# Kernel optimization log

Hardware: AMD Instinct MI355X
Metric: run time of the kernel (lower is better)

Reference implementation:

```python
import jax, jax.numpy as jnp
import numpy as np

B, T, D, OUT = 128, 4096, 64, 512  # batch(list len), max frames, feature_size, output_size


def setup_inputs() -> dict:
    key = jax.random.key(0)
    ks = jax.random.split(key, 12)
    s = 0.05
    return {
        "x": jax.random.normal(ks[0], (B, T, D), jnp.float32),
        # true frame counts per ragged item, in [256, T]
        "lengths": jax.random.randint(ks[1], (B,), 256, T + 1, dtype=jnp.int32),
        # td1: Conv2d(1, D, (3, D)) weight [D,1,3,D], bias [D]
        "W1": jax.random.normal(ks[2], (D, 1, 3, D), jnp.float32) * s,
        "b1": jax.random.normal(ks[3], (D,), jnp.float32) * s,
        # td2: Conv2d(1, D, (1, D)) weight [D,1,1,D], bias [D]
        "W2": jax.random.normal(ks[4], (D, 1, 1, D), jnp.float32) * s,
        "b2": jax.random.normal(ks[5], (D,), jnp.float32) * s,
        # segment-level MLP: D->256->256->OUT (torch Linear layout [out,in])
        "Wl1": jax.random.normal(ks[6], (256, D), jnp.float32) * s,
        "bl1": jax.random.normal(ks[7], (256,), jnp.float32) * s,
        "Wl2": jax.random.normal(ks[8], (256, 256), jnp.float32) * s,
        "bl2": jax.random.normal(ks[9], (256,), jnp.float32) * s,
        "Wl3": jax.random.normal(ks[10], (OUT, 256), jnp.float32) * s,
        "bl3": jax.random.normal(ks[11], (OUT,), jnp.float32) * s,
    }


def reference(x, lengths, W1, b1, W2, b2, Wl1, bl1, Wl2, bl2, Wl3, bl3):
    # td1: sliding window of 3 frames, full-width feature contraction -> [B, T-2, F]
    # (avoid materializing [B,T-2,3,D] windows; 3 shifted matmuls instead)
    w1 = W1[:, 0]  # [F, 3, D]
    h = b1
    for k in range(3):  # fixed tiny kernel width
        h = h + jnp.einsum('btd,fd->btf', x[:, k:T - 2 + k], w1[:, k])
    h = jax.nn.relu(h)
    # td2: context 0 -> per-frame linear F->F
    h = jnp.einsum('btf,gf->btg', h, W2[:, 0, 0]) + b2  # [B, T-2, F]
    # masked mean over valid frames (each item has lengths[i]-2 conv outputs)
    nvalid = (lengths - 2).astype(h.dtype)  # [B]
    mask = (jnp.arange(T - 2)[None, :] < (lengths - 2)[:, None]).astype(h.dtype)
    pooled = jnp.einsum('btg,bt->bg', h, mask) / nvalid[:, None]  # [B, F]
    # segment-level MLP
    z = jax.nn.relu(pooled @ Wl1.T + bl1)
    z = jax.nn.relu(z @ Wl2.T + bl2)
    return z @ Wl3.T + bl3  # [B, OUT]
```

## Files before the change

kernel.cpp:

```cpp
#include <hip/hip_runtime.h>
#include <hip/hip_bf16.h>

#define NB 128
#define NT 4096
#define ND 64
#define NTOUT 4094

typedef __attribute__((ext_vector_type(8))) short bf16x8;
typedef __attribute__((ext_vector_type(4))) float f32x4;

__device__ __forceinline__ short bfb(float f) {
    __hip_bfloat16 h = __float2bfloat16(f);
    return __builtin_bit_cast(short, h);
}

__device__ __forceinline__ bf16x8 pack8(f32x4 a, f32x4 b) {
    bf16x8 r;
    r[0] = bfb(a[0]); r[1] = bfb(a[1]); r[2] = bfb(a[2]); r[3] = bfb(a[3]);
    r[4] = bfb(b[0]); r[5] = bfb(b[1]); r[6] = bfb(b[2]); r[7] = bfb(b[3]);
    return r;
}

__global__ __launch_bounds__(256) void conv_pool_kernel(
    const float* __restrict__ x, const int* __restrict__ lengths,
    const float* __restrict__ W1, const float* __restrict__ b1,
    float* __restrict__ s_ws)
{
    const int b     = blockIdx.x >> 4;
    const int chunk = blockIdx.x & 15;
    const int nvalid = lengths[b] - 2;
    if (chunk * 256 >= nvalid) return;

    const int lane = threadIdx.x & 63;
    const int wave = threadIdx.x >> 6;
    const int lrow = lane & 15;
    const int lkg  = lane >> 4;

    bf16x8 wfrag[4][6];
    #pragma unroll
    for (int nt = 0; nt < 4; ++nt) {
        const float* wp = W1 + (nt * 16 + lrow) * 192 + lkg * 8;
        #pragma unroll
        for (int kk = 0; kk < 6; ++kk) {
            f32x4 w0 = *reinterpret_cast<const f32x4*>(wp + kk * 32);
            f32x4 w1v = *reinterpret_cast<const f32x4*>(wp + kk * 32 + 4);
            wfrag[nt][kk] = pack8(w0, w1v);
        }
    }
    float b1f[4];
    #pragma unroll
    for (int nt = 0; nt < 4; ++nt) b1f[nt] = b1[nt * 16 + lrow];

    float sums[4][4];
    #pragma unroll
    for (int nt = 0; nt < 4; ++nt)
        #pragma unroll
        for (int r = 0; r < 4; ++r) sums[nt][r] = 0.f;

    const float* xb = x + (size_t)b * (NT * ND);
    const int t_wave = chunk * 256 + wave * 64;

    for (int i = 0; i < 4; ++i) {
        const int t0 = t_wave + i * 16;
        int trow = t0 + lrow;
        int tload = trow > (NT - 3) ? (NT - 3) : trow;
        const float* ap = xb + (size_t)tload * ND + lkg * 8;

        bf16x8 afrag[6];
        #pragma unroll
        for (int kk = 0; kk < 6; ++kk) {
            f32x4 a0 = *reinterpret_cast<const f32x4*>(ap + kk * 32);
            f32x4 a1 = *reinterpret_cast<const f32x4*>(ap + kk * 32 + 4);
            afrag[kk] = pack8(a0, a1);
        }

        f32x4 acc[4];
        #pragma unroll
        for (int nt = 0; nt < 4; ++nt) acc[nt] = (f32x4){0.f, 0.f, 0.f, 0.f};

        #pragma unroll
        for (int kk = 0; kk < 6; ++kk) {
            #pragma unroll
            for (int nt = 0; nt < 4; ++nt)
                acc[nt] = __builtin_amdgcn_mfma_f32_16x16x32_bf16(
                    afrag[kk], wfrag[nt][kk], acc[nt], 0, 0, 0);
        }

        #pragma unroll
        for (int r = 0; r < 4; ++r) {
            const int tg = t0 + lkg * 4 + r;
            const bool valid = tg < nvalid;
            #pragma unroll
            for (int nt = 0; nt < 4; ++nt) {
                float v = acc[nt][r] + b1f[nt];
                v = fmaxf(v, 0.f);
                sums[nt][r] += valid ? v : 0.f;
            }
        }
    }

    #pragma unroll
    for (int nt = 0; nt < 4; ++nt) {
        float v = sums[nt][0] + sums[nt][1] + sums[nt][2] + sums[nt][3];
        v += __shfl_xor(v, 16, 64);
        v += __shfl_xor(v, 32, 64);
        if (lane < 16) atomicAdd(&s_ws[b * ND + nt * 16 + lane], v);
    }
}

__global__ __launch_bounds__(256) void mlp_kernel(
    const float* __restrict__ s_ws, const int* __restrict__ lengths,
    const float* __restrict__ W2, const float* __restrict__ b2,
    const float* __restrict__ Wl1, const float* __restrict__ bl1,
    const float* __restrict__ Wl2, const float* __restrict__ bl2,
    const float* __restrict__ Wl3, const float* __restrict__ bl3,
    float* __restrict__ out)
{
    __shared__ float sh_s[64], sh_p[64], sh_z1[256], sh_z2[256];
    const int b = blockIdx.x, tid = threadIdx.x;

    if (tid < 64) {
        float nv = (float)(lengths[b] - 2);
        sh_s[tid] = s_ws[b * 64 + tid] / nv;
    }
    __syncthreads();

    if (tid < 64) {
        float acc = b2[tid];
        const f32x4* wr = reinterpret_cast<const f32x4*>(W2 + tid * 64);
        const f32x4* vr = reinterpret_cast<const f32x4*>(sh_s);
        #pragma unroll 4
        for (int k = 0; k < 16; ++k) {
            f32x4 w = wr[k], v = vr[k];
            acc += w[0]*v[0] + w[1]*v[1] + w[2]*v[2] + w[3]*v[3];
        }
        sh_p[tid] = acc;
    }
    __syncthreads();

    {
        float acc = bl1[tid];
        const f32x4* wr = reinterpret_cast<const f32x4*>(Wl1 + tid * 64);
        const f32x4* vr = reinterpret_cast<const f32x4*>(sh_p);
        #pragma unroll 4
        for (int k = 0; k < 16; ++k) {
            f32x4 w = wr[k], v = vr[k];
            acc += w[0]*v[0] + w[1]*v[1] + w[2]*v[2] + w[3]*v[3];
        }
        sh_z1[tid] = fmaxf(acc, 0.f);
    }
    __syncthreads();

    {
        float acc = bl2[tid];
        const f32x4* wr = reinterpret_cast<const f32x4*>(Wl2 + tid * 256);
        const f32x4* vr = reinterpret_cast<const f32x4*>(sh_z1);
        #pragma unroll 4
        for (int k = 0; k < 64; ++k) {
            f32x4 w = wr[k], v = vr[k];
            acc += w[0]*v[0] + w[1]*v[1] + w[2]*v[2] + w[3]*v[3];
        }
        sh_z2[tid] = fmaxf(acc, 0.f);
    }
    __syncthreads();

    for (int o = tid; o < 512; o += 256) {
        float acc = bl3[o];
        const f32x4* wr = reinterpret_cast<const f32x4*>(Wl3 + o * 256);
        const f32x4* vr = reinterpret_cast<const f32x4*>(sh_z2);
        #pragma unroll 4
        for (int k = 0; k < 64; ++k) {
            f32x4 w = wr[k], v = vr[k];
            acc += w[0]*v[0] + w[1]*v[1] + w[2]*v[2] + w[3]*v[3];
        }
        out[(size_t)b * 512 + o] = acc;
    }
}

extern "C" void kernel_launch(void* const* d_in, const int* in_sizes, int n_in,
                              void* d_out, int out_size, void* d_ws, size_t ws_size,
                              hipStream_t stream) {
    const float* x       = (const float*)d_in[0];
    const int*   lengths = (const int*)d_in[1];
    const float* W1      = (const float*)d_in[2];
    const float* b1      = (const float*)d_in[3];
    const float* W2      = (const float*)d_in[4];
    const float* b2      = (const float*)d_in[5];
    const float* Wl1     = (const float*)d_in[6];
    const float* bl1     = (const float*)d_in[7];
    const float* Wl2     = (const float*)d_in[8];
    const float* bl2     = (const float*)d_in[9];
    const float* Wl3     = (const float*)d_in[10];
    const float* bl3     = (const float*)d_in[11];
    float* out = (float*)d_out;

    float* s_ws = (float*)d_ws;
    hipMemsetAsync(s_ws, 0, NB * ND * sizeof(float), stream);

    conv_pool_kernel<<<dim3(NB * 16), dim3(256), 0, stream>>>(x, lengths, W1, b1, s_ws);
    mlp_kernel<<<dim3(NB), dim3(256), 0, stream>>>(s_ws, lengths, W2, b2,
                                                   Wl1, bl1, Wl2, bl2, Wl3, bl3, out);
}
```

Measured before the change: 306.1 us.

## Stage x tiles in LDS via async global-to-LDS loads and prepack W1 once

The conv+pool kernel now copies each 130-row x tile into swizzled shared memory using global_load_lds. The three shifted windows then read the tile from LDS instead of re-reading overlapping rows from global memory. Chunks shrink to 128 frames with 32 blocks per item, per-wave partial sums are reduced in LDS before a single atomic per feature, and a separate setup kernel converts W1 to bf16 fragments once. The MLP kernel also uses vector accumulators with two partial sums. This adds a kernel launch and LDS pressure in exchange for less global traffic and fewer atomics.

```diff
diff --git a/kernel.cpp b/kernel.cpp
--- a/kernel.cpp
+++ b/kernel.cpp
@@ -4,7 +4,9 @@
 #define NB 128
 #define NT 4096
 #define ND 64
-#define NTOUT 4094
+#define CH 128
+#define NCHUNK 32
+#define NSEGS 33
 
 typedef __attribute__((ext_vector_type(8))) short bf16x8;
 typedef __attribute__((ext_vector_type(4))) float f32x4;
@@ -21,95 +23,124 @@
     return r;
 }
 
+__global__ void setup_kernel(const float* __restrict__ W1, short* __restrict__ wb) {
+    int idx = blockIdx.x * 256 + threadIdx.x;
+    if (idx >= 4 * 6 * 64) return;
+    int lane = idx & 63;
+    int kk   = (idx >> 6) % 6;
+    int nt   = idx / (6 * 64);
+    const float* wp = W1 + (nt * 16 + (lane & 15)) * 192 + (lane >> 4) * 8 + kk * 32;
+    bf16x8 r;
+    #pragma unroll
+    for (int j = 0; j < 8; ++j) r[j] = bfb(wp[j]);
+    reinterpret_cast<bf16x8*>(wb)[idx] = r;
+}
+
 __global__ __launch_bounds__(256) void conv_pool_kernel(
     const float* __restrict__ x, const int* __restrict__ lengths,
-    const float* __restrict__ W1, const float* __restrict__ b1,
-    float* __restrict__ s_ws)
+    const short* __restrict__ wb, const float* __restrict__ b1,
+    float* __restrict__ s_sum)
 {
-    const int b     = blockIdx.x >> 4;
-    const int chunk = blockIdx.x & 15;
+    __shared__ float lds[NSEGS * 256];
+    __shared__ float sh_red[4 * 64];
+
+    const int b      = blockIdx.x >> 5;
+    const int chunk  = blockIdx.x & (NCHUNK - 1);
     const int nvalid = lengths[b] - 2;
-    if (chunk * 256 >= nvalid) return;
+    const int t0     = chunk * CH;
+    if (t0 >= nvalid) return;
 
     const int lane = threadIdx.x & 63;
     const int wave = threadIdx.x >> 6;
     const int lrow = lane & 15;
     const int lkg  = lane >> 4;
 
-    bf16x8 wfrag[4][6];
-    #pragma unroll
-    for (int nt = 0; nt < 4; ++nt) {
-        const float* wp = W1 + (nt * 16 + lrow) * 192 + lkg * 8;
-        #pragma unroll
-        for (int kk = 0; kk < 6; ++kk) {
-            f32x4 w0 = *reinterpret_cast<const f32x4*>(wp + kk * 32);
-            f32x4 w1v = *reinterpret_cast<const f32x4*>(wp + kk * 32 + 4);
-            wfrag[nt][kk] = pack8(w0, w1v);
-        }
-    }
-    float b1f[4];
-    #pragma unroll
-    for (int nt = 0; nt < 4; ++nt) b1f[nt] = b1[nt * 16 + lrow];
-
-    float sums[4][4];
-    #pragma unroll
-    for (int nt = 0; nt < 4; ++nt)
-        #pragma unroll
-        for (int r = 0; r < 4; ++r) sums[nt][r] = 0.f;
-
+    const int rows_needed = min(CH + 2, nvalid - t0 + 2);
     const float* xb = x + (size_t)b * (NT * ND);
-    const int t_wave = chunk * 256 + wave * 64;
-
-    for (int i = 0; i < 4; ++i) {
-        const int t0 = t_wave + i * 16;
-        int trow = t0 + lrow;
-        int tload = trow > (NT - 3) ? (NT - 3) : trow;
-        const float* ap = xb + (size_t)tload * ND + lkg * 8;
-
-        bf16x8 afrag[6];
-        #pragma unroll
-        for (int kk = 0; kk < 6; ++kk) {
-            f32x4 a0 = *reinterpret_cast<const f32x4*>(ap + kk * 32);
-            f32x4 a1 = *reinterpret_cast<const f32x4*>(ap + kk * 32 + 4);
-            afrag[kk] = pack8(a0, a1);
-        }
-
-        f32x4 acc[4];
-        #pragma unroll
-        for (int nt = 0; nt < 4; ++nt) acc[nt] = (f32x4){0.f, 0.f, 0.f, 0.f};
-
-        #pragma unroll
-        for (int kk = 0; kk < 6; ++kk) {
-            #pragma unroll
-            for (int nt = 0; nt < 4; ++nt)
-                acc[nt] = __builtin_amdgcn_mfma_f32_16x16x32_bf16(
-                    afrag[kk], wfrag[nt][kk], acc[nt], 0, 0, 0);
-        }
-
-        #pragma unroll
-        for (int r = 0; r < 4; ++r) {
-            const int tg = t0 + lkg * 4 + r;
-            const bool valid = tg < nvalid;
-            #pragma unroll
-            for (int nt = 0; nt < 4; ++nt) {
-                float v = acc[nt][r] + b1f[nt];
-                v = fmaxf(v, 0.f);
-                sums[nt][r] += valid ? v : 0.f;
+
+    {
+        const int unit = lane & 15;
+        const int rl4  = lane >> 4;
+        for (int s = wave; s < NSEGS; s += 4) {
+            if (s * 4 < rows_needed) {
+                int row_local = s * 4 + rl4;
+                int rg = t0 + row_local; if (rg > NT - 1) rg = NT - 1;
+                int su = unit ^ (row_local & 7);
+                const float* src = xb + (size_t)rg * ND + su * 4;
+                __builtin_amdgcn_global_load_lds(
+                    (const __attribute__((address_space(1))) void*)src,
+                    (__attribute__((address_space(3))) void*)&lds[s * 256],
+                    16, 0, 0);
             }
         }
     }
 
+    bf16x8 wfrag[4][6];
+    #pragma unroll
+    for (int nt = 0; nt < 4; ++nt)
+        #pragma unroll
+        for (int kk = 0; kk < 6; ++kk)
+            wfrag[nt][kk] = reinterpret_cast<const bf16x8*>(wb)[(nt * 6 + kk) * 64 + lane];
+    float b1f[4];
+    #pragma unroll
+    for (int nt = 0; nt < 4; ++nt) b1f[nt] = b1[nt * 16 + lrow];
+
+    __syncthreads();
+
+    float sums[4] = {0.f, 0.f, 0.f, 0.f};
+
+    #pragma unroll
+    for (int i = 0; i < 2; ++i) {
+        const int tile = wave + i * 4;
+        const int tl0  = tile * 16;
+        if (t0 + tl0 < nvalid) {
+            f32x4 acc[4];
+            #pragma unroll
+            for (int nt = 0; nt < 4; ++nt) acc[nt] = (f32x4){0.f, 0.f, 0.f, 0.f};
+
+            #pragma unroll
+            for (int kk = 0; kk < 6; ++kk) {
+                const int xrl = tl0 + lrow + (kk >> 1);
+                const int e   = lkg * 2 + (kk & 1) * 8;
+                const int sw  = xrl & 7;
+                f32x4 a0 = *reinterpret_cast<const f32x4*>(&lds[xrl * 64 + ((e ^ sw) << 2)]);
+                f32x4 a1 = *reinterpret_cast<const f32x4*>(&lds[xrl * 64 + (((e + 1) ^ sw) << 2)]);
+                bf16x8 afrag = pack8(a0, a1);
+                #pragma unroll
+                for (int nt = 0; nt < 4; ++nt)
+                    acc[nt] = __builtin_amdgcn_mfma_f32_16x16x32_bf16(
+                        afrag, wfrag[nt][kk], acc[nt], 0, 0, 0);
+            }
+
+            #pragma unroll
+            for (int r = 0; r < 4; ++r) {
+                const bool valid = (t0 + tl0 + lkg * 4 + r) < nvalid;
+                #pragma unroll
+                for (int nt = 0; nt < 4; ++nt) {
+                    float v = fmaxf(acc[nt][r] + b1f[nt], 0.f);
+                    if (valid) sums[nt] += v;
+                }
+            }
+        }
+    }
+
     #pragma unroll
     for (int nt = 0; nt < 4; ++nt) {
-        float v = sums[nt][0] + sums[nt][1] + sums[nt][2] + sums[nt][3];
+        float v = sums[nt];
         v += __shfl_xor(v, 16, 64);
         v += __shfl_xor(v, 32, 64);
-        if (lane < 16) atomicAdd(&s_ws[b * ND + nt * 16 + lane], v);
+        if (lane < 16) sh_red[wave * 64 + nt * 16 + lane] = v;
+    }
+    __syncthreads();
+    if (threadIdx.x < 64) {
+        float tot = sh_red[threadIdx.x] + sh_red[64 + threadIdx.x] +
+                    sh_red[128 + threadIdx.x] + sh_red[192 + threadIdx.x];
+        atomicAdd(&s_sum[b * 64 + threadIdx.x], tot);
     }
 }
 
 __global__ __launch_bounds__(256) void mlp_kernel(
-    const float* __restrict__ s_ws, const int* __restrict__ lengths,
+    const float* __restrict__ s_sum, const int* __restrict__ lengths,
     const float* __restrict__ W2, const float* __restrict__ b2,
     const float* __restrict__ Wl1, const float* __restrict__ bl1,
     const float* __restrict__ Wl2, const float* __restrict__ bl2,
@@ -119,61 +150,50 @@
     __shared__ float sh_s[64], sh_p[64], sh_z1[256], sh_z2[256];
     const int b = blockIdx.x, tid = threadIdx.x;
 
+    if (tid < 64)
+        sh_s[tid] = s_sum[b * 64 + tid] / (float)(lengths[b] - 2);
+    __syncthreads();
+
     if (tid < 64) {
-        float nv = (float)(lengths[b] - 2);
-        sh_s[tid] = s_ws[b * 64 + tid] / nv;
-    }
-    __syncthreads();
-
-    if (tid < 64) {
-        float acc = b2[tid];
+        f32x4 acc = {0.f, 0.f, 0.f, 0.f};
         const f32x4* wr = reinterpret_cast<const f32x4*>(W2 + tid * 64);
         const f32x4* vr = reinterpret_cast<const f32x4*>(sh_s);
-        #pragma unroll 4
-        for (int k = 0; k < 16; ++k) {
-            f32x4 w = wr[k], v = vr[k];
-            acc += w[0]*v[0] + w[1]*v[1] + w[2]*v[2] + w[3]*v[3];
-        }
-        sh_p[tid] = acc;
-    }
-    __syncthreads();
-
-    {
-        float acc = bl1[tid];
+        #pragma unroll
+        for (int k = 0; k < 16; ++k) acc += wr[k] * vr[k];
+        sh_p[tid] = b2[tid] + acc[0] + acc[1] + acc[2] + acc[3];
+    }
+    __syncthreads();
+
+    {
+        f32x4 acc = {0.f, 0.f, 0.f, 0.f};
         const f32x4* wr = reinterpret_cast<const f32x4*>(Wl1 + tid * 64);
         const f32x4* vr = reinterpret_cast<const f32x4*>(sh_p);
-        #pragma unroll 4
-        for (int k = 0; k < 16; ++k) {
-            f32x4 w = wr[k], v = vr[k];
-            acc += w[0]*v[0] + w[1]*v[1] + w[2]*v[2] + w[3]*v[3];
-        }
-        sh_z1[tid] = fmaxf(acc, 0.f);
-    }
-    __syncthreads();
-
-    {
-        float acc = bl2[tid];
+        #pragma unroll
+        for (int k = 0; k < 16; ++k) acc += wr[k] * vr[k];
+        sh_z1[tid] = fmaxf(bl1[tid] + acc[0] + acc[1] + acc[2] + acc[3], 0.f);
+    }
+    __syncthreads();
+
+    {
+        f32x4 a0 = {0.f, 0.f, 0.f, 0.f}, a1 = {0.f, 0.f, 0.f, 0.f};
         const f32x4* wr = reinterpret_cast<const f32x4*>(Wl2 + tid * 256);
         const f32x4* vr = reinterpret_cast<const f32x4*>(sh_z1);
-        #pragma unroll 4
-        for (int k = 0; k < 64; ++k) {
-            f32x4 w = wr[k], v = vr[k];
-            acc += w[0]*v[0] + w[1]*v[1] + w[2]*v[2] + w[3]*v[3];
-        }
-        sh_z2[tid] = fmaxf(acc, 0.f);
-    }
-    __syncthreads();
-
-    for (int o = tid; o < 512; o += 256) {
-        float acc = bl3[o];
-        const f32x4* wr = reinterpret_cast<const f32x4*>(Wl3 + o * 256);
+        #pragma unroll
+        for (int k = 0; k < 64; k += 2) { a0 += wr[k] * vr[k]; a1 += wr[k + 1] * vr[k + 1]; }
+        f32x4 a = a0 + a1;
+        sh_z2[tid] = fmaxf(bl2[tid] + a[0] + a[1] + a[2] + a[3], 0.f);
+    }
+    __syncthreads();
+
+    {
+        f32x4 a0 = {0.f, 0.f, 0.f, 0.f}, a1 = {0.f, 0.f, 0.f, 0.f};
+        const f32x4* w0 = reinterpret_cast<const f32x4*>(Wl3 + (size_t)tid * 256);
+        const f32x4* w1 = reinterpret_cast<const f32x4*>(Wl3 + (size_t)(tid + 256) * 256);
         const f32x4* vr = reinterpret_cast<const f32x4*>(sh_z2);
-        #pragma unroll 4
-        for (int k = 0; k < 64; ++k) {
-            f32x4 w = wr[k], v = vr[k];
-            acc += w[0]*v[0] + w[1]*v[1] + w[2]*v[2] + w[3]*v[3];
-        }
-        out[(size_t)b * 512 + o] = acc;
+        #pragma unroll
+        for (int k = 0; k < 64; ++k) { a0 += w0[k] * vr[k]; a1 += w1[k] * vr[k]; }
+        out[(size_t)b * 512 + tid]       = bl3[tid]       + a0[0] + a0[1] + a0[2] + a0[3];
+        out[(size_t)b * 512 + 256 + tid] = bl3[tid + 256] + a1[0] + a1[1] + a1[2] + a1[3];
     }
 }
 
@@ -194,10 +214,12 @@
     const float* bl3     = (const float*)d_in[11];
     float* out = (float*)d_out;
 
-    float* s_ws = (float*)d_ws;
-    hipMemsetAsync(s_ws, 0, NB * ND * sizeof(float), stream);
-
-    conv_pool_kernel<<<dim3(NB * 16), dim3(256), 0, stream>>>(x, lengths, W1, b1, s_ws);
-    mlp_kernel<<<dim3(NB), dim3(256), 0, stream>>>(s_ws, lengths, W2, b2,
+    float* s_sum = (float*)d_ws;
+    short* wb    = (short*)((char*)d_ws + NB * ND * 4);
+
+    hipMemsetAsync(s_sum, 0, NB * ND * sizeof(float), stream);
+    setup_kernel<<<dim3(6), dim3(256), 0, stream>>>(W1, wb);
+    conv_pool_kernel<<<dim3(NB * NCHUNK), dim3(256), 0, stream>>>(x, lengths, wb, b1, s_sum);
+    mlp_kernel<<<dim3(NB), dim3(256), 0, stream>>>(s_sum, lengths, W2, b2,
                                                    Wl1, bl1, Wl2, bl2, Wl3, bl3, out);
 }
```

Measured after the change: 245.5 us. 19.8% less time.
